# Kernel tuning notes

Hardware: AMD Instinct MI355X
Metric: run time of the kernel (lower is better)

The kernel has to match this reference:

```python
import jax, jax.numpy as jnp
import numpy as np

W_SZ = 5          # fine_window_size
D_F = 128         # fine d_model
D_C = 256         # coarse d_model


def _unfold(x, W, stride):
    # x: [B, C, H, Wd] -> [B, L, W*W, C], matching torch F.unfold + reshape/permute
    B, C, H, Wd = x.shape
    p = W // 2
    xp = jnp.pad(x, ((0, 0), (0, 0), (p, p), (p, p)))
    Hc = (H + 2 * p - W) // stride + 1
    Wc = (Wd + 2 * p - W) // stride + 1
    ri = (jnp.arange(Hc) * stride)[:, None] + jnp.arange(W)          # [Hc, W]
    ci = (jnp.arange(Wc) * stride)[:, None] + jnp.arange(W)          # [Wc, W]
    # gather -> [B, C, Hc, W, Wc, W]
    patches = xp[:, :, ri[:, :, None, None], ci[None, None, :, :]]
    # -> [B, Hc, Wc, W, W, C] -> [B, L, W*W, C]
    patches = patches.transpose(0, 2, 4, 3, 5, 1)
    return patches.reshape(B, Hc * Wc, W * W, C)


def setup_inputs() -> dict:
    key = jax.random.key(0)
    ks = jax.random.split(key, 10)
    B, Hf, Wf = 2, 240, 320
    L = 4800  # 60*80 coarse cells
    M = 3000
    inp = {
        "feat_f0": jax.random.normal(ks[0], (B, D_F, Hf, Wf), jnp.float32),
        "feat_f1": jax.random.normal(ks[1], (B, D_F, Hf, Wf), jnp.float32),
        "feat_c0": jax.random.normal(ks[2], (B, L, D_C), jnp.float32),
        "feat_c1": jax.random.normal(ks[3], (B, L, D_C), jnp.float32),
        "hw0_f": 240,
        "hw0_c": 60,
        "b_ids": jax.random.randint(ks[4], (M,), 0, B, jnp.int64 if jax.config.jax_enable_x64 else jnp.int32),
        "i_ids": jax.random.randint(ks[5], (M,), 0, L, jnp.int64 if jax.config.jax_enable_x64 else jnp.int32),
        "j_ids": jax.random.randint(ks[6], (M,), 0, L, jnp.int64 if jax.config.jax_enable_x64 else jnp.int32),
        # Linear params, torch convention: y = x @ W.T + b
        "down_W": jax.random.normal(ks[7], (D_F, D_C), jnp.float32) * (2.0 / D_C) ** 0.5,
        "down_b": jnp.zeros((D_F,), jnp.float32),
        "merge_W": jax.random.normal(ks[8], (D_F, 2 * D_F), jnp.float32) * (1.0 / D_F) ** 0.5,
        "merge_b": jnp.zeros((D_F,), jnp.float32),
    }
    return inp


def reference(feat_f0, feat_f1, feat_c0, feat_c1, hw0_f, hw0_c,
              b_ids, i_ids, j_ids, down_W, down_b, merge_W, merge_b):
    W = W_SZ
    stride = hw0_f // hw0_c  # python int -> static
    # unfold both fine maps -> [B, L, W^2, d_f]
    f0_unf = _unfold(feat_f0, W, stride)
    f1_unf = _unfold(feat_f1, W, stride)
    # gather per-match windows -> [M, W^2, d_f]
    f0_win = f0_unf[b_ids, i_ids]
    f1_win = f1_unf[b_ids, j_ids]
    # coarse feats per match, concat along match dim -> [2M, d_c]
    c_cat = jnp.concatenate([feat_c0[b_ids, i_ids], feat_c1[b_ids, j_ids]], axis=0)
    c_win = c_cat @ down_W.T + down_b                                   # [2M, d_f]
    f_cat = jnp.concatenate([f0_win, f1_win], axis=0)                   # [2M, W^2, d_f]
    c_rep = jnp.broadcast_to(c_win[:, None, :], f_cat.shape)            # [2M, W^2, d_f]
    merged = jnp.concatenate([f_cat, c_rep], axis=-1) @ merge_W.T + merge_b
    M = b_ids.shape[0]
    return merged[:M], merged[M:]
```

## Files before the change

### kernel.cpp

```cpp
#include <hip/hip_runtime.h>


#define HF 240
#define WF 320
#define HWF (HF * WF)
#define LPOS 4800

typedef short short8 __attribute__((ext_vector_type(8)));
typedef float f32x4 __attribute__((ext_vector_type(4)));

__device__ __forceinline__ unsigned short f2bf(float x) {
  union { float f; unsigned u; } v; v.f = x;
  unsigned r = v.u + 0x7FFF + ((v.u >> 16) & 1);
  return (unsigned short)(r >> 16);
}

__global__ __launch_bounds__(256) void transpose_kernel(
    const float* __restrict__ f0, const float* __restrict__ f1,
    unsigned short* __restrict__ t0, unsigned short* __restrict__ t1) {
  __shared__ unsigned short tile[128][66];
  const int t = threadIdx.x;
  const int hw0 = blockIdx.x * 64;
  const int map = blockIdx.y;
  const float* src = ((map >> 1) ? f1 : f0) + (size_t)(map & 1) * 128 * HWF;
  unsigned short* dst = ((map >> 1) ? t1 : t0) + (size_t)(map & 1) * HWF * 128;

  const int p0 = (t & 31) * 2;
  const int cg = t >> 5;
  #pragma unroll
  for (int ci = 0; ci < 16; ++ci) {
    int c = ci * 8 + cg;
    float2 v = *(const float2*)&src[(size_t)c * HWF + hw0 + p0];
    ushort2 u;
    u.x = f2bf(v.x);
    u.y = f2bf(v.y);
    *(ushort2*)&tile[c][p0] = u;
  }
  __syncthreads();
  const int c4 = (t & 31) * 4;
  #pragma unroll
  for (int wi = 0; wi < 8; ++wi) {
    int p = wi * 8 + cg;
    ushort4 u;
    u.x = tile[c4 + 0][p];
    u.y = tile[c4 + 1][p];
    u.z = tile[c4 + 2][p];
    u.w = tile[c4 + 3][p];
    *(ushort4*)&dst[(size_t)(hw0 + p) * 128 + c4] = u;
  }
}

__global__ __launch_bounds__(256) void prep_kernel(
    const float* __restrict__ down_W, const float* __restrict__ down_b,
    const float* __restrict__ merge_W, const float* __restrict__ merge_b,
    float* __restrict__ CW, float* __restrict__ cbias,
    unsigned short* __restrict__ W1bf) {
  int idx = blockIdx.x * 256 + threadIdx.x;
  if (idx < 32768) {
    int k = idx >> 7, o = idx & 127;
    float s = 0.f;
    #pragma unroll 4
    for (int t = 0; t < 128; ++t)
      s += down_W[t * 256 + k] * merge_W[o * 256 + 128 + t];
    CW[idx] = s;
  } else if (idx < 49152) {
    int i2 = idx - 32768;
    int n = i2 >> 7, c = i2 & 127;
    W1bf[i2] = f2bf(merge_W[n * 256 + c]);
  } else if (idx < 49280) {
    int o = idx - 49152;
    float s = merge_b[o];
    #pragma unroll 4
    for (int t = 0; t < 128; ++t)
      s += down_b[t] * merge_W[o * 256 + 128 + t];
    cbias[o] = s;
  }
}

__global__ __launch_bounds__(256) void t2_kernel(
    const float* __restrict__ c0, const float* __restrict__ c1,
    const int* __restrict__ b_ids, const int* __restrict__ i_ids,
    const int* __restrict__ j_ids,
    const float* __restrict__ CW, const float* __restrict__ cbias,
    float* __restrict__ t2, int M) {
  __shared__ float crow[8][256];
  const int t = threadIdx.x;
  const int m0 = blockIdx.x * 8;
  const int M2 = 2 * M;
  #pragma unroll
  for (int it = 0; it < 8; ++it) {
    int m = m0 + it;
    float v = 0.f;
    if (m < M2) {
      int b, pos;
      const float* src;
      if (m < M) { b = b_ids[m]; pos = i_ids[m]; src = c0; }
      else       { b = b_ids[m - M]; pos = j_ids[m - M]; src = c1; }
      v = src[((size_t)b * LPOS + pos) * 256 + t];
    }
    crow[it][t] = v;
  }
  __syncthreads();
  const int o = t & 127, half = t >> 7;
  const int r0 = half * 4;
  float a0 = 0.f, a1 = 0.f, a2 = 0.f, a3 = 0.f;
  #pragma unroll 4
  for (int k = 0; k < 256; ++k) {
    float wv = CW[k * 128 + o];
    a0 += crow[r0 + 0][k] * wv;
    a1 += crow[r0 + 1][k] * wv;
    a2 += crow[r0 + 2][k] * wv;
    a3 += crow[r0 + 3][k] * wv;
  }
  const float cb = cbias[o];
  if (m0 + r0 + 0 < M2) t2[(size_t)(m0 + r0 + 0) * 128 + o] = a0 + cb;
  if (m0 + r0 + 1 < M2) t2[(size_t)(m0 + r0 + 1) * 128 + o] = a1 + cb;
  if (m0 + r0 + 2 < M2) t2[(size_t)(m0 + r0 + 2) * 128 + o] = a2 + cb;
  if (m0 + r0 + 3 < M2) t2[(size_t)(m0 + r0 + 3) * 128 + o] = a3 + cb;
}

__global__ __launch_bounds__(256) void fine_mfma_kernel(
    const unsigned short* __restrict__ t0, const unsigned short* __restrict__ t1,
    const int* __restrict__ b_ids, const int* __restrict__ i_ids,
    const int* __restrict__ j_ids,
    const unsigned short* __restrict__ W1bf, const float* __restrict__ t2,
    float* __restrict__ out, int M) {
  __shared__ unsigned short Bl[128 * 128];
  const int t = threadIdx.x;

  #pragma unroll
  for (int it = 0; it < 8; ++it) {
    int q = it * 256 + t;
    int n = q >> 4;
    int kb16 = (q & 15) * 16;
    short8 v = *(const short8*)&W1bf[n * 128 + (q & 15) * 8];
    int dstB = n * 256 + (kb16 ^ ((n & 7) << 4));
    *(short8*)((char*)Bl + dstB) = v;
  }

  const int wid = t >> 6, lane = t & 63;
  const int lr = lane & 15, lg = lane >> 4;
  const int m = blockIdx.x * 4 + wid;
  const int M2 = 2 * M;
  const bool active = (m < M2);

  short8 a[2][4];
  short8 az = {};
  if (active) {
    int b, pos;
    const unsigned short* tm;
    if (m < M) { b = b_ids[m]; pos = i_ids[m]; tm = t0; }
    else       { int mm = m - M; b = b_ids[mm]; pos = j_ids[mm]; tm = t1; }
    int hc = pos / 80, wc = pos - hc * 80;
    int h0 = hc * 4 - 2, w0 = wc * 4 - 2;
    #pragma unroll
    for (int mt = 0; mt < 2; ++mt) {
      int p = mt * 16 + lr;
      int pr = p / 5;
      int hh = h0 + pr, ww = w0 + (p - pr * 5);
      bool valid = (p < 25) && ((unsigned)hh < (unsigned)HF) && ((unsigned)ww < (unsigned)WF);
      if (!valid) { hh = 0; ww = 0; }
      const unsigned short* rowp =
          tm + (((size_t)b * HWF + (size_t)(hh * WF + ww)) << 7) + lg * 8;
      #pragma unroll
      for (int kk = 0; kk < 4; ++kk)
        a[mt][kk] = valid ? *(const short8*)(rowp + kk * 32) : az;
    }
  } else {
    #pragma unroll
    for (int mt = 0; mt < 2; ++mt)
      #pragma unroll
      for (int kk = 0; kk < 4; ++kk) a[mt][kk] = az;
  }

  __syncthreads();
  if (!active) return;

  f32x4 acc[2][8];
  #pragma unroll
  for (int mt = 0; mt < 2; ++mt)
    #pragma unroll
    for (int nt = 0; nt < 8; ++nt) {
      f32x4 z = {0.f, 0.f, 0.f, 0.f};
      acc[mt][nt] = z;
    }

  #pragma unroll
  for (int nt = 0; nt < 8; ++nt) {
    int n = nt * 16 + lr;
    int kbase = n * 256;
    int sw = (n & 7) << 4;
    short8 bfr[4];
    #pragma unroll
    for (int kk = 0; kk < 4; ++kk) {
      int kb = (kk * 64 + lg * 16) ^ sw;
      bfr[kk] = *(const short8*)((const char*)Bl + kbase + kb);
    }
    #pragma unroll
    for (int kk = 0; kk < 4; ++kk) {
      acc[0][nt] = __builtin_amdgcn_mfma_f32_16x16x32_bf16(a[0][kk], bfr[kk], acc[0][nt], 0, 0, 0);
      acc[1][nt] = __builtin_amdgcn_mfma_f32_16x16x32_bf16(a[1][kk], bfr[kk], acc[1][nt], 0, 0, 0);
    }
  }

  const float* t2row = t2 + (size_t)m * 128;
  float* orow = out + (size_t)m * 25 * 128;
  #pragma unroll
  for (int nt = 0; nt < 8; ++nt) {
    int o = nt * 16 + lr;
    float tv = t2row[o];
    #pragma unroll
    for (int mt = 0; mt < 2; ++mt) {
      #pragma unroll
      for (int j = 0; j < 4; ++j) {
        int r = mt * 16 + lg * 4 + j;
        if (r < 25) orow[r * 128 + o] = acc[mt][nt][j] + tv;
      }
    }
  }
}

extern "C" void kernel_launch(void* const* d_in, const int* in_sizes, int n_in,
                              void* d_out, int out_size, void* d_ws, size_t ws_size,
                              hipStream_t stream) {
  const float* f0      = (const float*)d_in[0];
  const float* f1      = (const float*)d_in[1];
  const float* c0      = (const float*)d_in[2];
  const float* c1      = (const float*)d_in[3];
  const int*   b_ids   = (const int*)d_in[6];
  const int*   i_ids   = (const int*)d_in[7];
  const int*   j_ids   = (const int*)d_in[8];
  const float* down_W  = (const float*)d_in[9];
  const float* down_b  = (const float*)d_in[10];
  const float* merge_W = (const float*)d_in[11];
  const float* merge_b = (const float*)d_in[12];
  const int M = in_sizes[6];
  const int M2 = 2 * M;

  char* wsb = (char*)d_ws;
  float* CW    = (float*)wsb;
  float* cbias = (float*)(wsb + 131072);
  float* t2    = (float*)(wsb + 131584);
  size_t t2_bytes = (size_t)M2 * 128 * 4;
  size_t off = 131584 + t2_bytes;
  off = (off + 255) & ~(size_t)255;
  unsigned short* W1bf = (unsigned short*)(wsb + off);
  off += 32768;
  unsigned short* t0 = (unsigned short*)(wsb + off);
  off += (size_t)2 * HWF * 128 * 2;
  unsigned short* t1 = (unsigned short*)(wsb + off);

  transpose_kernel<<<dim3(1200, 4), 256, 0, stream>>>(f0, f1, t0, t1);
  prep_kernel<<<193, 256, 0, stream>>>(down_W, down_b, merge_W, merge_b,
                                       CW, cbias, W1bf);
  t2_kernel<<<(M2 + 7) / 8, 256, 0, stream>>>(c0, c1, b_ids, i_ids, j_ids,
                                              CW, cbias, t2, M);
  fine_mfma_kernel<<<(M2 + 3) / 4, 256, 0, stream>>>(t0, t1, b_ids, i_ids, j_ids,
                                                     W1bf, t2, (float*)d_out, M);
}
```

Measured before the change: 107.4 us.

## Store transposed fine maps in channel-blocked [C/8][HW][8] bf16 layout

The fine feature maps were previously converted into a pixel-major [HW][128] bf16 layout. They are now converted into a channel-blocked layout with 16 blocks of 8 channels, each block stored as [HW][8]. The transpose kernel reads wide float4 rows over 1024 pixels and 16 channels and writes 16-byte vectors per pixel. The MFMA kernel's A-fragment gather is updated to index the new layout, so each lane fetches 16 bytes from separate channel planes rather than from one contiguous 256-byte pixel row. This makes the transpose cheaper but trades contiguous per-pixel reads in the gather for strided plane accesses.

```diff
diff --git a/kernel.cpp b/kernel.cpp
--- a/kernel.cpp
+++ b/kernel.cpp
@@ -7,6 +7,7 @@
 #define LPOS 4800
 
 typedef short short8 __attribute__((ext_vector_type(8)));
+typedef unsigned short ushort8 __attribute__((ext_vector_type(8)));
 typedef float f32x4 __attribute__((ext_vector_type(4)));
 
 __device__ __forceinline__ unsigned short f2bf(float x) {
@@ -18,35 +19,35 @@
 __global__ __launch_bounds__(256) void transpose_kernel(
     const float* __restrict__ f0, const float* __restrict__ f1,
     unsigned short* __restrict__ t0, unsigned short* __restrict__ t1) {
-  __shared__ unsigned short tile[128][66];
+  __shared__ unsigned short tile[16][1024];
   const int t = threadIdx.x;
-  const int hw0 = blockIdx.x * 64;
-  const int map = blockIdx.y;
-  const float* src = ((map >> 1) ? f1 : f0) + (size_t)(map & 1) * 128 * HWF;
-  unsigned short* dst = ((map >> 1) ? t1 : t0) + (size_t)(map & 1) * HWF * 128;
-
-  const int p0 = (t & 31) * 2;
-  const int cg = t >> 5;
-  #pragma unroll
-  for (int ci = 0; ci < 16; ++ci) {
-    int c = ci * 8 + cg;
-    float2 v = *(const float2*)&src[(size_t)c * HWF + hw0 + p0];
-    ushort2 u;
-    u.x = f2bf(v.x);
-    u.y = f2bf(v.y);
-    *(ushort2*)&tile[c][p0] = u;
+  const int hw0 = blockIdx.x * 1024;
+  const int cg = blockIdx.y;
+  const int mb = blockIdx.z;
+  const float* src = ((mb >> 1) ? f1 : f0)
+                   + ((size_t)(mb & 1) * 128 + (size_t)cg * 16) * HWF + hw0;
+  unsigned short* dst = ((mb >> 1) ? t1 : t0)
+                      + (((size_t)(mb & 1) * 16 + (size_t)cg * 2) * HWF + hw0) * 8;
+
+  #pragma unroll
+  for (int it = 0; it < 16; ++it) {
+    int q = it * 256 + t;
+    int ch = q >> 8, p4 = q & 255;
+    float4 v = *(const float4*)&src[(size_t)ch * HWF + p4 * 4];
+    ushort4 u;
+    u.x = f2bf(v.x); u.y = f2bf(v.y); u.z = f2bf(v.z); u.w = f2bf(v.w);
+    *(ushort4*)&tile[ch][p4 * 4] = u;
   }
   __syncthreads();
-  const int c4 = (t & 31) * 4;
-  #pragma unroll
-  for (int wi = 0; wi < 8; ++wi) {
-    int p = wi * 8 + cg;
-    ushort4 u;
-    u.x = tile[c4 + 0][p];
-    u.y = tile[c4 + 1][p];
-    u.z = tile[c4 + 2][p];
-    u.w = tile[c4 + 3][p];
-    *(ushort4*)&dst[(size_t)(hw0 + p) * 128 + c4] = u;
+
+  #pragma unroll
+  for (int it = 0; it < 8; ++it) {
+    int q = it * 256 + t;
+    int cb = q >> 10, p = q & 1023;
+    ushort8 v;
+    #pragma unroll
+    for (int j = 0; j < 8; ++j) v[j] = tile[cb * 8 + j][p];
+    *(ushort8*)&dst[((size_t)cb * HWF + p) * 8] = v;
   }
 }
 
@@ -151,6 +152,7 @@
     const unsigned short* tm;
     if (m < M) { b = b_ids[m]; pos = i_ids[m]; tm = t0; }
     else       { int mm = m - M; b = b_ids[mm]; pos = j_ids[mm]; tm = t1; }
+    tm += (size_t)b * 16 * HWF * 8;
     int hc = pos / 80, wc = pos - hc * 80;
     int h0 = hc * 4 - 2, w0 = wc * 4 - 2;
     #pragma unroll
@@ -159,12 +161,13 @@
       int pr = p / 5;
       int hh = h0 + pr, ww = w0 + (p - pr * 5);
       bool valid = (p < 25) && ((unsigned)hh < (unsigned)HF) && ((unsigned)ww < (unsigned)WF);
-      if (!valid) { hh = 0; ww = 0; }
-      const unsigned short* rowp =
-          tm + (((size_t)b * HWF + (size_t)(hh * WF + ww)) << 7) + lg * 8;
+      int px = valid ? (hh * WF + ww) : 0;
       #pragma unroll
-      for (int kk = 0; kk < 4; ++kk)
-        a[mt][kk] = valid ? *(const short8*)(rowp + kk * 32) : az;
+      for (int kk = 0; kk < 4; ++kk) {
+        const short8* ap =
+            (const short8*)(tm + (((size_t)(kk * 4 + lg) * HWF + px) << 3));
+        a[mt][kk] = valid ? *ap : az;
+      }
     }
   } else {
     #pragma unroll
@@ -241,16 +244,15 @@
   float* CW    = (float*)wsb;
   float* cbias = (float*)(wsb + 131072);
   float* t2    = (float*)(wsb + 131584);
-  size_t t2_bytes = (size_t)M2 * 128 * 4;
-  size_t off = 131584 + t2_bytes;
+  size_t off = 131584 + (size_t)M2 * 128 * 4;
   off = (off + 255) & ~(size_t)255;
   unsigned short* W1bf = (unsigned short*)(wsb + off);
   off += 32768;
   unsigned short* t0 = (unsigned short*)(wsb + off);
-  off += (size_t)2 * HWF * 128 * 2;
+  off += (size_t)2 * 16 * HWF * 8 * 2;
   unsigned short* t1 = (unsigned short*)(wsb + off);
 
-  transpose_kernel<<<dim3(1200, 4), 256, 0, stream>>>(f0, f1, t0, t1);
+  transpose_kernel<<<dim3(75, 8, 4), 256, 0, stream>>>(f0, f1, t0, t1);
   prep_kernel<<<193, 256, 0, stream>>>(down_W, down_b, merge_W, merge_b,
                                        CW, cbias, W1bf);
   t2_kernel<<<(M2 + 7) / 8, 256, 0, stream>>>(c0, c1, b_ids, i_ids, j_ids,
```

Result: slower. 112.5 us (+4.7%).
